# Performance work log

Hardware: AMD Instinct MI355X
Metric: run time of the kernel (lower is better)

## Reference

```python
import jax, jax.numpy as jnp
import numpy as np

N = 100000       # nodes
E = 1600000      # edges
F_IN = 128       # input features
HID = 64         # hidden dim
CLS = 16         # classes


def setup_inputs() -> dict:
    key = jax.random.key(0)
    k = jax.random.split(key, 6)
    x = jax.random.normal(k[0], (N, F_IN), dtype=jnp.float32)
    src = jax.random.randint(k[1], (E,), 0, N, dtype=jnp.int32)
    dst = jax.random.randint(k[2], (E,), 0, N, dtype=jnp.int32)
    edge_index = jnp.stack([src, dst], axis=0)
    W1 = jax.random.normal(k[3], (F_IN, HID), dtype=jnp.float32) * (1.0 / np.sqrt(F_IN))
    b1 = jnp.zeros((HID,), dtype=jnp.float32)
    W2 = jax.random.normal(k[4], (HID, CLS), dtype=jnp.float32) * (1.0 / np.sqrt(HID))
    b2 = jnp.zeros((CLS,), dtype=jnp.float32)
    return {"x": x, "edge_index": edge_index, "W1": W1, "b1": b1, "W2": W2, "b2": b2}


def gcn_conv(x, W, b, src, dst, n_nodes):
    # GCNConv(normalize=True): h = W x; out_i = sum_{j->i} h_j / sqrt(d_i d_j) + h_i / d_i + b
    # (self-loops added with weight 1; deg includes the self-loop)
    h = x @ W                                             # [N, out]
    ones = jnp.ones(src.shape[0], dtype=x.dtype)
    deg = jax.ops.segment_sum(ones, dst, num_segments=n_nodes) + 1.0   # [N]
    dinv = deg ** -0.5
    norm = dinv[src] * dinv[dst]                          # [E]
    msg = h[src] * norm[:, None]                          # [E, out] gather
    out = jax.ops.segment_sum(msg, dst, num_segments=n_nodes)          # scatter-add
    out = out + h * (1.0 / deg)[:, None] + b              # self-loop term + bias
    return out


def reference(x, edge_index, W1, b1, W2, b2):
    src, dst = edge_index[0], edge_index[1]
    n = x.shape[0]
    h = jax.nn.relu(gcn_conv(x, W1, b1, src, dst, n))
    # dropout(p=0.5) is identity in eval mode
    h = jax.nn.relu(gcn_conv(h, W2, b2, src, dst, n))
    return jax.nn.log_softmax(h, axis=-1)
```

## Files before the change

kernel.cpp:

```cpp
#include <hip/hip_runtime.h>
#include <hip/hip_bf16.h>


typedef unsigned short u16;
typedef __attribute__((ext_vector_type(8))) short short8;
typedef __attribute__((ext_vector_type(4))) float f32x4;

#define CAP 4096

__device__ __forceinline__ float bf2f(u16 u) {
  return __uint_as_float(((unsigned int)u) << 16);
}
__device__ __forceinline__ u16 f2bf(float f) {
  unsigned int u = __float_as_uint(f);
  u += 0x7fffu + ((u >> 16) & 1u);
  return (u16)(u >> 16);
}
__device__ __forceinline__ float blo(unsigned int u) {
  return __uint_as_float(u << 16);
}
__device__ __forceinline__ float bhi(unsigned int u) {
  return __uint_as_float(u & 0xffff0000u);
}

__global__ __launch_bounds__(512) void kpartc(
    const int* __restrict__ src, const int* __restrict__ dst,
    int* __restrict__ cursor, int* __restrict__ etmp,
    const void* __restrict__ W1r, const void* __restrict__ b1r,
    const void* __restrict__ W2r, const void* __restrict__ b2r,
    u16* __restrict__ W1b, float* __restrict__ b1f, u16* __restrict__ W2b,
    float* __restrict__ b2f, int* __restrict__ mode, int E, int NB) {
  __shared__ int hist[1024], basep[1024];
  __shared__ float red[8];
  __shared__ int smode;
  int tid = threadIdx.x;

  if (blockIdx.x == 0) {
    const u16* w = (const u16*)W1r;
    float mx = 0.f;
    for (int i = tid; i < 8192; i += 512) {
      float av = fabsf(bf2f(w[i]));
      if (!(av <= 1e6f)) av = 3e38f;
      mx = fmaxf(mx, av);
    }
    #pragma unroll
    for (int off = 32; off >= 1; off >>= 1) mx = fmaxf(mx, __shfl_xor(mx, off, 64));
    if ((tid & 63) == 0) red[tid >> 6] = mx;
    __syncthreads();
    if (tid == 0) {
      float m2 = 0.f;
      #pragma unroll
      for (int wv = 0; wv < 8; ++wv) m2 = fmaxf(m2, red[wv]);
      smode = (m2 > 1e6f) ? 1 : 0;
      mode[0] = smode;
    }
    __syncthreads();
    int m = smode;
    for (int i = tid; i < 8192; i += 512)
      W1b[i] = m ? f2bf(((const float*)W1r)[i]) : ((const u16*)W1r)[i];
    for (int i = tid; i < 1024; i += 512)
      W2b[i] = m ? f2bf(((const float*)W2r)[i]) : ((const u16*)W2r)[i];
    if (tid < 64) b1f[tid] = m ? ((const float*)b1r)[tid] : bf2f(((const u16*)b1r)[tid]);
    if (tid < 16) b2f[tid] = m ? ((const float*)b2r)[tid] : bf2f(((const u16*)b2r)[tid]);
    return;
  }

  for (int i = tid; i < 1024; i += 512) hist[i] = 0;
  __syncthreads();
  int e0 = (blockIdx.x - 1) * 8192 + tid * 16;
  int pk[16], off[16], cb[16];
  if (e0 + 15 < E) {
    int4 s4[4], d4[4];
    #pragma unroll
    for (int u = 0; u < 4; ++u) {
      s4[u] = ((const int4*)(src + e0))[u];
      d4[u] = ((const int4*)(dst + e0))[u];
    }
    const int* sp = (const int*)s4;
    const int* dp = (const int*)d4;
    #pragma unroll
    for (int k = 0; k < 16; ++k) {
      int s = sp[k], d = dp[k];
      cb[k] = d >> 7;
      pk[k] = (s << 7) | (d & 127);
      off[k] = atomicAdd(&hist[cb[k]], 1);
    }
  } else {
    #pragma unroll
    for (int k = 0; k < 16; ++k) {
      int e = e0 + k;
      cb[k] = -1;
      if (e < E) {
        int s = src[e], d = dst[e];
        cb[k] = d >> 7;
        pk[k] = (s << 7) | (d & 127);
        off[k] = atomicAdd(&hist[cb[k]], 1);
      }
    }
  }
  __syncthreads();
  for (int i = tid; i < NB; i += 512)
    if (hist[i]) basep[i] = atomicAdd(&cursor[i], hist[i]);
  __syncthreads();
  if (e0 + 15 < E) {
    #pragma unroll
    for (int k = 0; k < 16; ++k)
      etmp[cb[k] * CAP + basep[cb[k]] + off[k]] = pk[k];
  } else {
    #pragma unroll
    for (int k = 0; k < 16; ++k)
      if (cb[k] >= 0) etmp[cb[k] * CAP + basep[cb[k]] + off[k]] = pk[k];
  }
}

__global__ __launch_bounds__(512) void kgemm1f(
    const void* __restrict__ xraw, const u16* __restrict__ W1b,
    const int* __restrict__ mode, const int* __restrict__ etmp,
    const int* __restrict__ cursor, float* __restrict__ dinv,
    u16* __restrict__ h1s, int* __restrict__ esort, int2* __restrict__ rowse,
    int N) {
  __shared__ int eL[CAP];
  __shared__ int hist[128], curs[128];
  __shared__ float sdinv[128];
  int tid = threadIdx.x;
  int bk = blockIdx.x;
  int base = bk * CAP;
  int cnt = cursor[bk];
  int node0 = bk << 7;

  if (tid < 128) hist[tid] = 0;
  __syncthreads();
  for (int i = tid; i < cnt; i += 512) {
    int pk = etmp[base + i];
    eL[i] = pk;
    atomicAdd(&hist[pk & 127], 1);
  }
  __syncthreads();
  if (tid < 128) {
    float dv = rsqrtf((float)(hist[tid] + 1));
    sdinv[tid] = dv;
    int nd = node0 + tid;
    if (nd < N) dinv[nd] = dv;
  }
  if (tid < 64) {
    int v0 = hist[tid], v1 = hist[tid + 64];
    int s0 = v0;
    #pragma unroll
    for (int off = 1; off < 64; off <<= 1) {
      int t = __shfl_up(s0, off, 64);
      if (tid >= off) s0 += t;
    }
    int tot0 = __shfl(s0, 63, 64);
    int s1 = v1;
    #pragma unroll
    for (int off = 1; off < 64; off <<= 1) {
      int t = __shfl_up(s1, off, 64);
      if (tid >= off) s1 += t;
    }
    s1 += tot0;
    int e0x = s0 - v0, e1x = s1 - v1;
    curs[tid] = e0x;
    curs[tid + 64] = e1x;
    int n0 = node0 + tid, n1 = n0 + 64;
    if (n0 < N) rowse[n0] = make_int2(base + e0x, base + e0x + v0);
    if (n1 < N) rowse[n1] = make_int2(base + e1x, base + e1x + v1);
  }
  __syncthreads();
  for (int i = tid; i < cnt; i += 512) {
    int pk = eL[i];
    int pos = atomicAdd(&curs[pk & 127], 1);
    esort[base + pos] = pk >> 7;
  }

  int mflag = mode[0];
  int lane = tid & 63, wv = tid >> 6;
  int m = lane & 15, q = lane >> 4;
  int row0 = node0 + wv * 16;

  short8 bfrag[4][4];
  for (int jb = 0; jb < 4; ++jb)
    for (int kb = 0; kb < 4; ++kb) {
      short8 f;
      #pragma unroll
      for (int j = 0; j < 8; ++j)
        f[j] = (short)W1b[(kb * 32 + q * 8 + j) * 64 + jb * 16 + m];
      bfrag[jb][kb] = f;
    }

  f32x4 acc[4];
  #pragma unroll
  for (int jb = 0; jb < 4; ++jb) acc[jb] = (f32x4){0.f, 0.f, 0.f, 0.f};

  int rowm = row0 + m;
  size_t rc = (size_t)((rowm < N) ? rowm : (N - 1));
  #pragma unroll
  for (int kb = 0; kb < 4; ++kb) {
    short8 a;
    if (mflag) {
      const float* xf = (const float*)xraw + rc * 128 + kb * 32 + q * 8;
      float4 u0 = ((const float4*)xf)[0];
      float4 u1 = ((const float4*)xf)[1];
      __hip_bfloat162 p0 = __float22bfloat162_rn(make_float2(u0.x, u0.y));
      __hip_bfloat162 p1 = __float22bfloat162_rn(make_float2(u0.z, u0.w));
      __hip_bfloat162 p2 = __float22bfloat162_rn(make_float2(u1.x, u1.y));
      __hip_bfloat162 p3 = __float22bfloat162_rn(make_float2(u1.z, u1.w));
      unsigned int w0 = *(const unsigned int*)&p0;
      unsigned int w1 = *(const unsigned int*)&p1;
      unsigned int w2 = *(const unsigned int*)&p2;
      unsigned int w3 = *(const unsigned int*)&p3;
      a[0] = (short)(w0 & 0xffff); a[1] = (short)(w0 >> 16);
      a[2] = (short)(w1 & 0xffff); a[3] = (short)(w1 >> 16);
      a[4] = (short)(w2 & 0xffff); a[5] = (short)(w2 >> 16);
      a[6] = (short)(w3 & 0xffff); a[7] = (short)(w3 >> 16);
    } else {
      a = *(const short8*)((const u16*)xraw + rc * 128 + kb * 32 + q * 8);
    }
    #pragma unroll
    for (int jb = 0; jb < 4; ++jb)
      acc[jb] = __builtin_amdgcn_mfma_f32_16x16x32_bf16(a, bfrag[jb][kb], acc[jb], 0, 0, 0);
  }

  #pragma unroll
  for (int r = 0; r < 4; ++r) {
    int rr = row0 + q * 4 + r;
    if (rr < N) {
      float dv = sdinv[wv * 16 + q * 4 + r];
      #pragma unroll
      for (int jb = 0; jb < 4; ++jb)
        h1s[(size_t)rr * 64 + jb * 16 + m] = f2bf(acc[jb][r] * dv);
    }
  }
}

__global__ __launch_bounds__(256) void kagg1f(
    const u16* __restrict__ h1s, const int* __restrict__ esort,
    const int2* __restrict__ rowse, const float* __restrict__ dinv,
    const float* __restrict__ b1f, const u16* __restrict__ W2b,
    u16* __restrict__ h2sb, int N) {
  __shared__ __align__(16) u16 sA[4][16 * 72];
  __shared__ float sdv[4][16];
  int tid = threadIdx.x;
  int lane = tid & 63, wv = tid >> 6;
  int o = lane >> 3, fl = lane & 7;
  int wbase = blockIdx.x * 64 + wv * 16;

  const uint4* __restrict__ h1v4 = (const uint4*)h1s;

  #pragma unroll
  for (int sub = 0; sub < 2; ++sub) {
    int nloc = sub * 8 + o;
    int node = wbase + nloc;
    int cn = (node < N) ? node : (N - 1);
    int2 se = (node < N) ? rowse[node] : make_int2(0, 0);
    int beg = se.x, end = se.y;
    float a0 = 0.f, a1 = 0.f, a2 = 0.f, a3 = 0.f;
    float a4 = 0.f, a5 = 0.f, a6 = 0.f, a7 = 0.f;

    int k = beg;
    int myi = (k + 8 <= end) ? esort[k + fl] : 0;
    while (k + 8 <= end) {
      int cur = myi;
      if (k + 16 <= end) myi = esort[k + 8 + fl];
      uint4 g[8];
      #pragma unroll
      for (int p = 0; p < 8; ++p) {
        int s = __shfl(cur, (o << 3) + p, 64);
        g[p] = h1v4[s * 8 + fl];
      }
      #pragma unroll
      for (int p = 0; p < 8; ++p) {
        a0 += blo(g[p].x); a1 += bhi(g[p].x);
        a2 += blo(g[p].y); a3 += bhi(g[p].y);
        a4 += blo(g[p].z); a5 += bhi(g[p].z);
        a6 += blo(g[p].w); a7 += bhi(g[p].w);
      }
      k += 8;
    }
    for (; k < end; ++k) {
      int s = esort[k];
      uint4 g = h1v4[s * 8 + fl];
      a0 += blo(g.x); a1 += bhi(g.x);
      a2 += blo(g.y); a3 += bhi(g.y);
      a4 += blo(g.z); a5 += bhi(g.z);
      a6 += blo(g.w); a7 += bhi(g.w);
    }

    uint4 sg = h1v4[cn * 8 + fl];
    float dv = dinv[cn];
    float4 bva = ((const float4*)b1f)[fl * 2];
    float4 bvb = ((const float4*)b1f)[fl * 2 + 1];
    float v0 = fmaxf(dv * (a0 + blo(sg.x)) + bva.x, 0.f);
    float v1 = fmaxf(dv * (a1 + bhi(sg.x)) + bva.y, 0.f);
    float v2 = fmaxf(dv * (a2 + blo(sg.y)) + bva.z, 0.f);
    float v3 = fmaxf(dv * (a3 + bhi(sg.y)) + bva.w, 0.f);
    float v4 = fmaxf(dv * (a4 + blo(sg.z)) + bvb.x, 0.f);
    float v5 = fmaxf(dv * (a5 + bhi(sg.z)) + bvb.y, 0.f);
    float v6 = fmaxf(dv * (a6 + blo(sg.w)) + bvb.z, 0.f);
    float v7 = fmaxf(dv * (a7 + bhi(sg.w)) + bvb.w, 0.f);
    uint4 st;
    st.x = (unsigned int)f2bf(v0) | ((unsigned int)f2bf(v1) << 16);
    st.y = (unsigned int)f2bf(v2) | ((unsigned int)f2bf(v3) << 16);
    st.z = (unsigned int)f2bf(v4) | ((unsigned int)f2bf(v5) << 16);
    st.w = (unsigned int)f2bf(v6) | ((unsigned int)f2bf(v7) << 16);
    *(uint4*)&sA[wv][nloc * 72 + fl * 8] = st;
    if (fl == 0) sdv[wv][nloc] = dv;
  }

  int m16 = lane & 15, q = lane >> 4;
  short8 bw0, bw1;
  #pragma unroll
  for (int j = 0; j < 8; ++j) {
    bw0[j] = (short)W2b[(q * 8 + j) * 16 + m16];
    bw1[j] = (short)W2b[(32 + q * 8 + j) * 16 + m16];
  }
  __builtin_amdgcn_wave_barrier();

  const u16* ar = &sA[wv][m16 * 72];
  short8 af0 = *(const short8*)(ar + q * 8);
  short8 af1 = *(const short8*)(ar + 32 + q * 8);
  f32x4 c = (f32x4){0.f, 0.f, 0.f, 0.f};
  c = __builtin_amdgcn_mfma_f32_16x16x32_bf16(af0, bw0, c, 0, 0, 0);
  c = __builtin_amdgcn_mfma_f32_16x16x32_bf16(af1, bw1, c, 0, 0, 0);
  #pragma unroll
  for (int r = 0; r < 4; ++r) {
    int nloc2 = q * 4 + r;
    int nd2 = wbase + nloc2;
    if (nd2 < N) h2sb[(size_t)nd2 * 16 + m16] = f2bf(c[r] * sdv[wv][nloc2]);
  }
}

__global__ __launch_bounds__(256) void kagg2(
    const u16* __restrict__ h2sb, const int* __restrict__ esort,
    const int2* __restrict__ rowse, const float* __restrict__ dinv,
    const float* __restrict__ b2f, const int* __restrict__ mode,
    void* __restrict__ out, int n) {
  int mflag = mode[0];
  int tid = threadIdx.x;
  int lane = tid & 63, wv = tid >> 6;
  int oc = lane >> 3, ol = lane & 7;
  int hl = ol >> 2, fl = ol & 3;
  int node = blockIdx.x * 32 + wv * 8 + oc;
  if (node >= n) node = n - 1;
  int2 se = rowse[node];
  int beg = se.x, end = se.y;
  const uint2* h2v = (const uint2*)h2sb;
  uint2 sg = h2v[node * 4 + fl];
  float a0 = 0.f, a1 = 0.f, a2 = 0.f, a3 = 0.f;

  int k = beg;
  for (; k + 8 <= end; k += 8) {
    int i0 = esort[k + hl], i1 = esort[k + 2 + hl];
    int i2 = esort[k + 4 + hl], i3 = esort[k + 6 + hl];
    uint2 g0 = h2v[i0 * 4 + fl];
    uint2 g1 = h2v[i1 * 4 + fl];
    uint2 g2 = h2v[i2 * 4 + fl];
    uint2 g3 = h2v[i3 * 4 + fl];
    a0 += bf2f((u16)(g0.x & 0xffff)) + bf2f((u16)(g1.x & 0xffff))
        + bf2f((u16)(g2.x & 0xffff)) + bf2f((u16)(g3.x & 0xffff));
    a1 += bf2f((u16)(g0.x >> 16)) + bf2f((u16)(g1.x >> 16))
        + bf2f((u16)(g2.x >> 16)) + bf2f((u16)(g3.x >> 16));
    a2 += bf2f((u16)(g0.y & 0xffff)) + bf2f((u16)(g1.y & 0xffff))
        + bf2f((u16)(g2.y & 0xffff)) + bf2f((u16)(g3.y & 0xffff));
    a3 += bf2f((u16)(g0.y >> 16)) + bf2f((u16)(g1.y >> 16))
        + bf2f((u16)(g2.y >> 16)) + bf2f((u16)(g3.y >> 16));
  }
  for (; k < end; k += 2) {
    int e = k + hl;
    bool valid = e < end;
    uint2 g = h2v[esort[valid ? e : (end - 1)] * 4 + fl];
    if (valid) {
      a0 += bf2f((u16)(g.x & 0xffff));  a1 += bf2f((u16)(g.x >> 16));
      a2 += bf2f((u16)(g.y & 0xffff));  a3 += bf2f((u16)(g.y >> 16));
    }
  }
  a0 += __shfl_xor(a0, 4, 8);  a1 += __shfl_xor(a1, 4, 8);
  a2 += __shfl_xor(a2, 4, 8);  a3 += __shfl_xor(a3, 4, 8);

  float dv = dinv[node];
  float4 bv = ((const float4*)b2f)[fl];
  float v0 = fmaxf(dv * (a0 + bf2f((u16)(sg.x & 0xffff))) + bv.x, 0.f);
  float v1 = fmaxf(dv * (a1 + bf2f((u16)(sg.x >> 16))) + bv.y, 0.f);
  float v2 = fmaxf(dv * (a2 + bf2f((u16)(sg.y & 0xffff))) + bv.z, 0.f);
  float v3 = fmaxf(dv * (a3 + bf2f((u16)(sg.y >> 16))) + bv.w, 0.f);

  float m = fmaxf(fmaxf(v0, v1), fmaxf(v2, v3));
  m = fmaxf(m, __shfl_xor(m, 1, 4));
  m = fmaxf(m, __shfl_xor(m, 2, 4));
  float ex = __expf(v0 - m) + __expf(v1 - m) + __expf(v2 - m) + __expf(v3 - m);
  ex += __shfl_xor(ex, 1, 4);
  ex += __shfl_xor(ex, 2, 4);
  float lg = __logf(ex);
  float r0 = v0 - m - lg, r1 = v1 - m - lg;
  float r2 = v2 - m - lg, r3 = v3 - m - lg;
  if (hl == 0) {
    if (mflag) {
      ((float4*)out)[(size_t)node * 4 + fl] = make_float4(r0, r1, r2, r3);
    } else {
      uint2 o;
      o.x = (unsigned int)f2bf(r0) | ((unsigned int)f2bf(r1) << 16);
      o.y = (unsigned int)f2bf(r2) | ((unsigned int)f2bf(r3) << 16);
      ((uint2*)out)[(size_t)node * 4 + fl] = o;
    }
  }
}

extern "C" void kernel_launch(void* const* d_in, const int* in_sizes, int n_in,
                              void* d_out, int out_size, void* d_ws, size_t ws_size,
                              hipStream_t stream) {
  const void* x  = d_in[0];
  const int* ei  = (const int*)d_in[1];
  const void* W1 = d_in[2];
  const void* b1 = d_in[3];
  const void* W2 = d_in[4];
  const void* b2 = d_in[5];

  const int N = in_sizes[0] / 128;
  const int E = in_sizes[1] / 2;
  const int* src = ei;
  const int* dst = ei + E;
  const int NB = (N + 127) >> 7;

  char* ws = (char*)d_ws;
  size_t off = 0;
  auto alloc = [&](size_t bytes) -> char* {
    char* p = ws + off;
    off = (off + bytes + 255) & ~(size_t)255;
    return p;
  };
  u16*   h1s    = (u16*)  alloc((size_t)N * 64 * 2);
  u16*   h2sb   = (u16*)  alloc((size_t)N * 16 * 2);
  int*   etmp   = (int*)  alloc((size_t)NB * CAP * 4);
  int*   esort  = (int*)  alloc((size_t)NB * CAP * 4);
  int2*  rowse  = (int2*) alloc((size_t)N * 8);
  float* dinv   = (float*)alloc((size_t)N * 4);
  int*   cursor = (int*)  alloc((size_t)NB * 4);
  u16*   W1b    = (u16*)  alloc(8192 * 2);
  u16*   W2b    = (u16*)  alloc(1024 * 2);
  float* b1f    = (float*)alloc(64 * 4);
  float* b2f    = (float*)alloc(16 * 4);
  int*   mode   = (int*)  alloc(4);

  hipMemsetAsync(cursor, 0, (size_t)NB * 4, stream);

  int pblocks = (E + 8191) / 8192;
  kpartc<<<pblocks + 1, 512, 0, stream>>>(src, dst, cursor, etmp,
                                          W1, b1, W2, b2,
                                          W1b, b1f, W2b, b2f, mode, E, NB);
  kgemm1f<<<NB, 512, 0, stream>>>(x, W1b, mode, etmp, cursor, dinv, h1s,
                                  esort, rowse, N);
  kagg1f<<<(N + 63) / 64, 256, 0, stream>>>(h1s, esort, rowse, dinv, b1f, W2b,
                                            h2sb, N);
  kagg2<<<(N + 31) / 32, 256, 0, stream>>>(h2sb, esort, rowse, dinv, b2f, mode,
                                           d_out, N);
}
```

Measured before the change: 198.4 us.

## Split bucket sort and GEMM into separate blocks, compute degrees with global atomics

Per-node degree counting moves into the partition kernel as global atomics, so the second kernel no longer rebuilds a shared-memory histogram. That kernel now runs bucket-sort blocks and GEMM blocks as independent 256-thread blocks (three per bucket), and the GEMM half reads dinv straight from the degree array. W1 is pre-permuted into MFMA fragment order so each lane loads its B fragment with one vector load instead of gathering scalar elements. The cost is 1.6M global atomics on deg plus an extra memset, in exchange for more parallelism and higher occupancy in the GEMM stage.

```diff
diff --git a/kernel.cpp b/kernel.cpp
--- a/kernel.cpp
+++ b/kernel.cpp
@@ -25,10 +25,10 @@
 
 __global__ __launch_bounds__(512) void kpartc(
     const int* __restrict__ src, const int* __restrict__ dst,
-    int* __restrict__ cursor, int* __restrict__ etmp,
+    int* __restrict__ cursor, int* __restrict__ etmp, int* __restrict__ deg,
     const void* __restrict__ W1r, const void* __restrict__ b1r,
     const void* __restrict__ W2r, const void* __restrict__ b2r,
-    u16* __restrict__ W1b, float* __restrict__ b1f, u16* __restrict__ W2b,
+    u16* __restrict__ W1t, float* __restrict__ b1f, u16* __restrict__ W2b,
     float* __restrict__ b2f, int* __restrict__ mode, int E, int NB) {
   __shared__ int hist[1024], basep[1024];
   __shared__ float red[8];
@@ -56,8 +56,13 @@
     }
     __syncthreads();
     int m = smode;
-    for (int i = tid; i < 8192; i += 512)
-      W1b[i] = m ? f2bf(((const float*)W1r)[i]) : ((const u16*)W1r)[i];
+    for (int i = tid; i < 8192; i += 512) {
+      int f = i >> 9, l = (i >> 3) & 63, j = i & 7;
+      int k = (f >> 2) * 32 + (l >> 4) * 8 + j;
+      int n = (f & 3) * 16 + (l & 15);
+      int s = k * 64 + n;
+      W1t[i] = m ? f2bf(((const float*)W1r)[s]) : ((const u16*)W1r)[s];
+    }
     for (int i = tid; i < 1024; i += 512)
       W2b[i] = m ? f2bf(((const float*)W2r)[i]) : ((const u16*)W2r)[i];
     if (tid < 64) b1f[tid] = m ? ((const float*)b1r)[tid] : bf2f(((const u16*)b1r)[tid]);
@@ -84,6 +89,7 @@
       cb[k] = d >> 7;
       pk[k] = (s << 7) | (d & 127);
       off[k] = atomicAdd(&hist[cb[k]], 1);
+      atomicAdd(&deg[d], 1);
     }
   } else {
     #pragma unroll
@@ -95,6 +101,7 @@
         cb[k] = d >> 7;
         pk[k] = (s << 7) | (d & 127);
         off[k] = atomicAdd(&hist[cb[k]], 1);
+        atomicAdd(&deg[d], 1);
       }
     }
   }
@@ -113,85 +120,67 @@
   }
 }
 
-__global__ __launch_bounds__(512) void kgemm1f(
-    const void* __restrict__ xraw, const u16* __restrict__ W1b,
+__global__ __launch_bounds__(256, 6) void kgemm1f(
+    const void* __restrict__ xraw, const u16* __restrict__ W1t,
     const int* __restrict__ mode, const int* __restrict__ etmp,
-    const int* __restrict__ cursor, float* __restrict__ dinv,
-    u16* __restrict__ h1s, int* __restrict__ esort, int2* __restrict__ rowse,
-    int N) {
-  __shared__ int eL[CAP];
-  __shared__ int hist[128], curs[128];
-  __shared__ float sdinv[128];
+    const int* __restrict__ cursor, const int* __restrict__ deg,
+    float* __restrict__ dinv, u16* __restrict__ h1s, int* __restrict__ esort,
+    int2* __restrict__ rowse, int N, int NB) {
   int tid = threadIdx.x;
-  int bk = blockIdx.x;
-  int base = bk * CAP;
-  int cnt = cursor[bk];
+  int bid = blockIdx.x;
+
+  if (bid < NB) {
+    __shared__ int curs[128];
+    int bk = bid;
+    int base = bk * CAP;
+    int cnt = cursor[bk];
+    int node0 = bk << 7;
+    if (tid < 64) {
+      int n0 = node0 + tid, n1 = n0 + 64;
+      int v0 = (n0 < N) ? deg[n0] : 0;
+      int v1 = (n1 < N) ? deg[n1] : 0;
+      int s0 = v0;
+      #pragma unroll
+      for (int off = 1; off < 64; off <<= 1) {
+        int t = __shfl_up(s0, off, 64);
+        if (tid >= off) s0 += t;
+      }
+      int tot0 = __shfl(s0, 63, 64);
+      int s1 = v1;
+      #pragma unroll
+      for (int off = 1; off < 64; off <<= 1) {
+        int t = __shfl_up(s1, off, 64);
+        if (tid >= off) s1 += t;
+      }
+      s1 += tot0;
+      int e0x = s0 - v0, e1x = s1 - v1;
+      curs[tid] = e0x;
+      curs[tid + 64] = e1x;
+      if (n0 < N) rowse[n0] = make_int2(base + e0x, base + e0x + v0);
+      if (n1 < N) rowse[n1] = make_int2(base + e1x, base + e1x + v1);
+    }
+    __syncthreads();
+    for (int i = tid; i < cnt; i += 256) {
+      int pk = etmp[base + i];
+      int pos = atomicAdd(&curs[pk & 127], 1);
+      esort[base + pos] = pk >> 7;
+    }
+    return;
+  }
+
+  int g = bid - NB;
+  int bk = g >> 1, half = g & 1;
   int node0 = bk << 7;
-
-  if (tid < 128) hist[tid] = 0;
-  __syncthreads();
-  for (int i = tid; i < cnt; i += 512) {
-    int pk = etmp[base + i];
-    eL[i] = pk;
-    atomicAdd(&hist[pk & 127], 1);
-  }
-  __syncthreads();
-  if (tid < 128) {
-    float dv = rsqrtf((float)(hist[tid] + 1));
-    sdinv[tid] = dv;
-    int nd = node0 + tid;
-    if (nd < N) dinv[nd] = dv;
-  }
-  if (tid < 64) {
-    int v0 = hist[tid], v1 = hist[tid + 64];
-    int s0 = v0;
-    #pragma unroll
-    for (int off = 1; off < 64; off <<= 1) {
-      int t = __shfl_up(s0, off, 64);
-      if (tid >= off) s0 += t;
-    }
-    int tot0 = __shfl(s0, 63, 64);
-    int s1 = v1;
-    #pragma unroll
-    for (int off = 1; off < 64; off <<= 1) {
-      int t = __shfl_up(s1, off, 64);
-      if (tid >= off) s1 += t;
-    }
-    s1 += tot0;
-    int e0x = s0 - v0, e1x = s1 - v1;
-    curs[tid] = e0x;
-    curs[tid + 64] = e1x;
-    int n0 = node0 + tid, n1 = n0 + 64;
-    if (n0 < N) rowse[n0] = make_int2(base + e0x, base + e0x + v0);
-    if (n1 < N) rowse[n1] = make_int2(base + e1x, base + e1x + v1);
-  }
-  __syncthreads();
-  for (int i = tid; i < cnt; i += 512) {
-    int pk = eL[i];
-    int pos = atomicAdd(&curs[pk & 127], 1);
-    esort[base + pos] = pk >> 7;
-  }
-
   int mflag = mode[0];
   int lane = tid & 63, wv = tid >> 6;
-  int m = lane & 15, q = lane >> 4;
-  int row0 = node0 + wv * 16;
-
-  short8 bfrag[4][4];
-  for (int jb = 0; jb < 4; ++jb)
-    for (int kb = 0; kb < 4; ++kb) {
-      short8 f;
-      #pragma unroll
-      for (int j = 0; j < 8; ++j)
-        f[j] = (short)W1b[(kb * 32 + q * 8 + j) * 64 + jb * 16 + m];
-      bfrag[jb][kb] = f;
-    }
+  int m16 = lane & 15, q = lane >> 4;
+  int row0 = node0 + half * 64 + wv * 16;
 
   f32x4 acc[4];
   #pragma unroll
   for (int jb = 0; jb < 4; ++jb) acc[jb] = (f32x4){0.f, 0.f, 0.f, 0.f};
 
-  int rowm = row0 + m;
+  int rowm = row0 + m16;
   size_t rc = (size_t)((rowm < N) ? rowm : (N - 1));
   #pragma unroll
   for (int kb = 0; kb < 4; ++kb) {
@@ -216,18 +205,27 @@
       a = *(const short8*)((const u16*)xraw + rc * 128 + kb * 32 + q * 8);
     }
     #pragma unroll
-    for (int jb = 0; jb < 4; ++jb)
-      acc[jb] = __builtin_amdgcn_mfma_f32_16x16x32_bf16(a, bfrag[jb][kb], acc[jb], 0, 0, 0);
-  }
-
+    for (int jb = 0; jb < 4; ++jb) {
+      short8 bwf = *(const short8*)(W1t + (size_t)((kb * 4 + jb) * 64 + lane) * 8);
+      acc[jb] = __builtin_amdgcn_mfma_f32_16x16x32_bf16(a, bwf, acc[jb], 0, 0, 0);
+    }
+  }
+
+  int r4 = row0 + q * 4;
+  int4 dg = *(const int4*)(deg + r4);
+  float dv[4];
+  dv[0] = rsqrtf((float)(dg.x + 1));
+  dv[1] = rsqrtf((float)(dg.y + 1));
+  dv[2] = rsqrtf((float)(dg.z + 1));
+  dv[3] = rsqrtf((float)(dg.w + 1));
   #pragma unroll
   for (int r = 0; r < 4; ++r) {
-    int rr = row0 + q * 4 + r;
+    int rr = r4 + r;
     if (rr < N) {
-      float dv = sdinv[wv * 16 + q * 4 + r];
+      if (m16 == 0) dinv[rr] = dv[r];
       #pragma unroll
       for (int jb = 0; jb < 4; ++jb)
-        h1s[(size_t)rr * 64 + jb * 16 + m] = f2bf(acc[jb][r] * dv);
+        h1s[(size_t)rr * 64 + jb * 16 + m16] = f2bf(acc[jb][r] * dv[r]);
     }
   }
 }
@@ -434,20 +432,22 @@
   int2*  rowse  = (int2*) alloc((size_t)N * 8);
   float* dinv   = (float*)alloc((size_t)N * 4);
   int*   cursor = (int*)  alloc((size_t)NB * 4);
-  u16*   W1b    = (u16*)  alloc(8192 * 2);
+  int*   deg    = (int*)  alloc((size_t)(N + 128) * 4);
+  u16*   W1t    = (u16*)  alloc(8192 * 2);
   u16*   W2b    = (u16*)  alloc(1024 * 2);
   float* b1f    = (float*)alloc(64 * 4);
   float* b2f    = (float*)alloc(16 * 4);
   int*   mode   = (int*)  alloc(4);
 
   hipMemsetAsync(cursor, 0, (size_t)NB * 4, stream);
+  hipMemsetAsync(deg, 0, (size_t)(N + 128) * 4, stream);
 
   int pblocks = (E + 8191) / 8192;
-  kpartc<<<pblocks + 1, 512, 0, stream>>>(src, dst, cursor, etmp,
+  kpartc<<<pblocks + 1, 512, 0, stream>>>(src, dst, cursor, etmp, deg,
                                           W1, b1, W2, b2,
-                                          W1b, b1f, W2b, b2f, mode, E, NB);
-  kgemm1f<<<NB, 512, 0, stream>>>(x, W1b, mode, etmp, cursor, dinv, h1s,
-                                  esort, rowse, N);
+                                          W1t, b1f, W2b, b2f, mode, E, NB);
+  kgemm1f<<<3 * NB, 256, 0, stream>>>(x, W1t, mode, etmp, cursor, deg, dinv,
+                                      h1s, esort, rowse, N, NB);
   kagg1f<<<(N + 63) / 64, 256, 0, stream>>>(h1s, esort, rowse, dinv, b1f, W2b,
                                             h2sb, N);
   kagg2<<<(N + 31) / 32, 256, 0, stream>>>(h2sb, esort, rowse, dinv, b2f, mode,
```

Measured after the change: 249.3 us. +25.7%, slower.
